# Optimization experiments

Hardware: AMD Instinct MI355X
Metric: run time of the kernel (lower is better)

The kernel has to match this reference:

```python
import jax, jax.numpy as jnp
import numpy as np
from jax import lax

THRESHOLD = 0.3  # nn.Threshold(threshold, 0): y = x if x > threshold else 0
KERNEL = 3       # 3x3 maxpool, stride 1, pad 1 (SAME)


def setup_inputs() -> dict:
    key = jax.random.key(0)
    # [B=1, C=7, H, W] raw feature map (pre-sigmoid logits) from the UNet head
    feature = jax.random.normal(key, (1, 7, 2048, 2048), dtype=jnp.float32)
    return {"feature": feature, "max_detections": 4096}


def reference(feature, max_detections):
    # split along channel dim: 5 keypoint heatmaps, 1 side logit, 1 size logit
    heatmap = feature[:, :5]   # [1,5,H,W]
    side = feature[:, 5:6]     # [1,1,H,W]
    sizes = feature[:, 6:7]    # [1,1,H,W]

    activated = jax.nn.sigmoid(heatmap)
    thresholded = jnp.where(activated > THRESHOLD, activated, jnp.zeros((), activated.dtype))
    # 3x3 stride-1 SAME maxpool (local-max NMS)
    pooled = lax.reduce_window(thresholded, -jnp.inf, lax.max,
                               (1, 1, KERNEL, KERNEL), (1, 1, 1, 1), 'SAME')
    peak_mask = (pooled == thresholded)
    masked = (thresholded * peak_mask.astype(thresholded.dtype))[0]  # [5,H,W]
    masked_bool = masked > 0                                          # [5,H,W]

    side_act = jax.nn.sigmoid(side)[0, 0]    # [H,W]
    sizes_act = jax.nn.sigmoid(sizes)[0, 0]  # [H,W]
    probs_full = jnp.max(activated[0], axis=0)  # [H,W] max over 5 channels

    # fixed-size nonzero (jit-shapeable equivalent of torch .nonzero()/masked_select;
    # entries past the true count are padded with index 0 and zeroed out)
    c, y, x = jnp.nonzero(masked_bool, size=max_detections, fill_value=0)
    n_valid = jnp.sum(masked_bool)
    valid = (jnp.arange(max_detections) < n_valid).astype(probs_full.dtype)

    coords = jnp.stack([c, y, x], axis=1)           # [K,3] like torch nonzero order
    probs = probs_full[y, x] * valid                # masked_select broadcasts [H,W] vs [5,H,W]
    size_width = sizes_act[y, x] * valid
    size_height = sizes_act[y, x] * valid
    side_sel = side_act[y, x] * valid
    return probs, coords, size_width, size_height, side_sel
```

## Files before the change

### kernel.cpp

```cpp
#include <hip/hip_runtime.h>
#include <stdint.h>
#include <math.h>

#define IMG_H 2048
#define IMG_W 2048
#define CH_PIX (IMG_H * IMG_W)
#define MAXDET 4096
#define R_PB 8
#define NBLK 1280

__device__ __forceinline__ float sigmoidf_(float v) {
    return 1.0f / (1.0f + expf(-v));
}
__device__ __forceinline__ float sigthr_(float v) {
    float a = 1.0f / (1.0f + expf(-v));
    return a > 0.3f ? a : 0.0f;
}
__device__ __forceinline__ float max3_(float a, float b, float c) {
    return fmaxf(fmaxf(a, b), c);
}

__global__ __launch_bounds__(256) void pass_a(const float* __restrict__ feat,
                                              uint8_t* __restrict__ mask_bytes,
                                              unsigned* __restrict__ counts) {
    int blk = blockIdx.x;
    int c = blk >> 8;
    int ytile = blk & 255;
    int y0 = ytile << 3;
    const float* chan = feat + (size_t)c * CH_PIX;
    int t = threadIdx.x;
    int lane = t & 63;
    int xb = t << 3;
    int xe = (lane == 0) ? (xb - 1) : (xb + 8);
    bool edge_lane = (lane == 0) || (lane == 63);
    bool edge_ok = edge_lane && ((unsigned)xe < (unsigned)IMG_W);

    float sp[8], sc[8], sn[8];
    float ep, ec, en;

    auto load8 = [&](int y, float* s, float& e) {
        if ((unsigned)y >= (unsigned)IMG_H) {
#pragma unroll
            for (int j = 0; j < 8; ++j) s[j] = 0.0f;
            e = 0.0f;
            return;
        }
        const float* row = chan + (size_t)y * IMG_W;
        float4 a = *(const float4*)(row + xb);
        float4 b = *(const float4*)(row + xb + 4);
        float rv = -INFINITY;
        if (edge_ok) rv = row[xe];
        s[0] = sigthr_(a.x); s[1] = sigthr_(a.y); s[2] = sigthr_(a.z); s[3] = sigthr_(a.w);
        s[4] = sigthr_(b.x); s[5] = sigthr_(b.y); s[6] = sigthr_(b.z); s[7] = sigthr_(b.w);
        e = sigthr_(rv);
    };

    load8(y0 - 1, sp, ep);
    load8(y0,     sc, ec);

    unsigned cnt = 0;
    size_t bb = (size_t)c * (CH_PIX / 8) + (size_t)y0 * (IMG_W / 8) + t;

    for (int r = 0; r < R_PB; ++r) {
        load8(y0 + r + 1, sn, en);
        float cm[8];
#pragma unroll
        for (int j = 0; j < 8; ++j) cm[j] = max3_(sp[j], sc[j], sn[j]);
        float cme = max3_(ep, ec, en);
        float cmL = __shfl_up(cm[7], 1, 64);
        float cmR = __shfl_down(cm[0], 1, 64);
        if (lane == 0)  cmL = cme;
        if (lane == 63) cmR = cme;
        unsigned byte = 0;
#pragma unroll
        for (int j = 0; j < 8; ++j) {
            float l  = j       ? cm[j - 1] : cmL;
            float rr = (j < 7) ? cm[j + 1] : cmR;
            float pooled = max3_(l, cm[j], rr);
            if (sc[j] > 0.0f && pooled == sc[j]) byte |= (1u << j);
        }
        mask_bytes[bb + (size_t)r * (IMG_W / 8)] = (uint8_t)byte;
        cnt += __popc(byte);
#pragma unroll
        for (int j = 0; j < 8; ++j) { sp[j] = sc[j]; sc[j] = sn[j]; }
        ep = ec; ec = en;
    }

#pragma unroll
    for (int off = 32; off; off >>= 1) cnt += __shfl_down(cnt, off, 64);
    __shared__ unsigned s4[4];
    if (lane == 0) s4[t >> 6] = cnt;
    __syncthreads();
    if (t == 0) counts[blk] = s4[0] + s4[1] + s4[2] + s4[3];
}

__global__ __launch_bounds__(256) void pass_b(const float* __restrict__ feat,
                                              const uint64_t* __restrict__ masks,
                                              const unsigned* __restrict__ counts,
                                              float* __restrict__ out) {
    int blk = blockIdx.x;
    int t = threadIdx.x;
    int wave = t >> 6, lane = t & 63;

    unsigned p_lt = 0, p_all = 0;
    for (int i = t; i < NBLK; i += 256) {
        unsigned v = counts[i];
        p_all += v;
        if (i < blk) p_lt += v;
    }
#pragma unroll
    for (int off = 32; off; off >>= 1) {
        p_lt  += __shfl_down(p_lt,  off, 64);
        p_all += __shfl_down(p_all, off, 64);
    }
    __shared__ unsigned sl[4], sa[4];
    if (lane == 0) { sl[wave] = p_lt; sa[wave] = p_all; }
    __syncthreads();
    unsigned boff  = sl[0] + sl[1] + sl[2] + sl[3];
    unsigned total = sa[0] + sa[1] + sa[2] + sa[3];

    if (blk == NBLK - 1) {
        unsigned start = total < MAXDET ? total : MAXDET;
        for (unsigned k = start + t; k < MAXDET; k += 256) {
            out[k] = 0.0f;
            out[MAXDET + 3 * k + 0] = 0.0f;
            out[MAXDET + 3 * k + 1] = 0.0f;
            out[MAXDET + 3 * k + 2] = 0.0f;
            out[4 * MAXDET + k] = 0.0f;
            out[5 * MAXDET + k] = 0.0f;
            out[6 * MAXDET + k] = 0.0f;
        }
    }
    if (boff >= MAXDET) return;

    uint64_t w = masks[(size_t)blk * 256 + t];
    unsigned cnt = (unsigned)__popcll(w);
    __shared__ unsigned tmp[256];
    __shared__ uint32_t det_lds[MAXDET];
    tmp[t] = cnt;
    __syncthreads();
    for (int off = 1; off < 256; off <<= 1) {
        unsigned u = (t >= off) ? tmp[t - off] : 0u;
        __syncthreads();
        tmp[t] += u;
        __syncthreads();
    }
    unsigned rank = boff + tmp[t] - cnt;
    unsigned bsum = tmp[255];
    uint32_t pbase = (uint32_t)blk * 16384u + (uint32_t)t * 64u;
    while (w) {
        int b = __ffsll((unsigned long long)w) - 1;
        w &= w - 1;
        if (rank < MAXDET) det_lds[rank - boff] = pbase + (uint32_t)b;
        rank++;
    }
    __syncthreads();

    unsigned nend = boff + bsum; if (nend > MAXDET) nend = MAXDET;
    unsigned nloc = nend - boff;
    for (unsigned k = t; k < nloc; k += 256) {
        uint32_t p = det_lds[k];
        unsigned rk = boff + k;
        int c = (int)(p >> 22);
        int rem = (int)(p & (CH_PIX - 1));
        int y = rem >> 11, x = rem & 2047;
        size_t pix = (size_t)y * IMG_W + x;
        float pm = sigmoidf_(feat[pix]);
#pragma unroll
        for (int ch = 1; ch < 5; ++ch)
            pm = fmaxf(pm, sigmoidf_(feat[(size_t)ch * CH_PIX + pix]));
        float sdv = sigmoidf_(feat[(size_t)5 * CH_PIX + pix]);
        float szv = sigmoidf_(feat[(size_t)6 * CH_PIX + pix]);
        out[rk] = pm;
        out[MAXDET + 3 * rk + 0] = (float)c;
        out[MAXDET + 3 * rk + 1] = (float)y;
        out[MAXDET + 3 * rk + 2] = (float)x;
        out[4 * MAXDET + rk] = szv;
        out[5 * MAXDET + rk] = szv;
        out[6 * MAXDET + rk] = sdv;
    }
}

extern "C" void kernel_launch(void* const* d_in, const int* in_sizes, int n_in,
                              void* d_out, int out_size, void* d_ws, size_t ws_size,
                              hipStream_t stream) {
    const float* feat = (const float*)d_in[0];
    float* out = (float*)d_out;
    uint8_t* mask_bytes = (uint8_t*)d_ws;
    unsigned* counts = (unsigned*)((char*)d_ws + (size_t)NBLK * 2048);

    pass_a<<<NBLK, 256, 0, stream>>>(feat, mask_bytes, counts);
    pass_b<<<NBLK, 256, 0, stream>>>(feat, (const uint64_t*)d_ws, counts, out);
}
```

Measured before the change: 183.2 us.

## Replace per-pixel sigmoid in NMS pass with raw-logit compare plus exact verify pass

```diff
diff --git a/kernel.cpp b/kernel.cpp
--- a/kernel.cpp
+++ b/kernel.cpp
@@ -6,8 +6,11 @@
 #define IMG_W 2048
 #define CH_PIX (IMG_H * IMG_W)
 #define MAXDET 4096
-#define R_PB 8
 #define NBLK 1280
+#define FRONTIER 8192
+#define CUT_LO (-0.8474f)
+#define CUT_HI (-0.8472f)
+#define DELTA  (1e-4f)
 
 __device__ __forceinline__ float sigmoidf_(float v) {
     return 1.0f / (1.0f + expf(-v));
@@ -18,55 +21,66 @@
 }
 __device__ __forceinline__ float max3_(float a, float b, float c) {
     return fmaxf(fmaxf(a, b), c);
+}
+__device__ __forceinline__ float maskv_(float v) {
+    return v > CUT_HI ? v : -INFINITY;
 }
 
 __global__ __launch_bounds__(256) void pass_a(const float* __restrict__ feat,
                                               uint8_t* __restrict__ mask_bytes,
                                               unsigned* __restrict__ counts) {
     int blk = blockIdx.x;
-    int c = blk >> 8;
-    int ytile = blk & 255;
+    int c = blk >> 8, ytile = blk & 255;
     int y0 = ytile << 3;
     const float* chan = feat + (size_t)c * CH_PIX;
-    int t = threadIdx.x;
-    int lane = t & 63;
+    int t = threadIdx.x, lane = t & 63;
     int xb = t << 3;
-    int xe = (lane == 0) ? (xb - 1) : (xb + 8);
-    bool edge_lane = (lane == 0) || (lane == 63);
-    bool edge_ok = edge_lane && ((unsigned)xe < (unsigned)IMG_W);
-
-    float sp[8], sc[8], sn[8];
-    float ep, ec, en;
-
-    auto load8 = [&](int y, float* s, float& e) {
+    int xe = (lane == 0) ? xb - 1 : xb + 8;
+    bool edge_ok = ((lane == 0) || (lane == 63)) && ((unsigned)xe < (unsigned)IMG_W);
+
+    auto load_raw = [&](int y, float* r, float& er) {
         if ((unsigned)y >= (unsigned)IMG_H) {
 #pragma unroll
-            for (int j = 0; j < 8; ++j) s[j] = 0.0f;
-            e = 0.0f;
+            for (int j = 0; j < 8; ++j) r[j] = -INFINITY;
+            er = -INFINITY;
             return;
         }
         const float* row = chan + (size_t)y * IMG_W;
         float4 a = *(const float4*)(row + xb);
         float4 b = *(const float4*)(row + xb + 4);
-        float rv = -INFINITY;
-        if (edge_ok) rv = row[xe];
-        s[0] = sigthr_(a.x); s[1] = sigthr_(a.y); s[2] = sigthr_(a.z); s[3] = sigthr_(a.w);
-        s[4] = sigthr_(b.x); s[5] = sigthr_(b.y); s[6] = sigthr_(b.z); s[7] = sigthr_(b.w);
-        e = sigthr_(rv);
+        r[0] = a.x; r[1] = a.y; r[2] = a.z; r[3] = a.w;
+        r[4] = b.x; r[5] = b.y; r[6] = b.z; r[7] = b.w;
+        er = edge_ok ? row[xe] : -INFINITY;
     };
 
-    load8(y0 - 1, sp, ep);
-    load8(y0,     sc, ec);
+    float pa[8], pb[8], pc[8];
+    float rb[8], rc[8], rn[8];
+    float ea, eb, ec, etmp;
+
+    load_raw(y0 - 1, rn, etmp);
+#pragma unroll
+    for (int j = 0; j < 8; ++j) pa[j] = maskv_(rn[j]);
+    ea = maskv_(etmp);
+    load_raw(y0, rb, etmp);
+#pragma unroll
+    for (int j = 0; j < 8; ++j) pb[j] = maskv_(rb[j]);
+    eb = maskv_(etmp);
+    load_raw(y0 + 1, rc, etmp);
+#pragma unroll
+    for (int j = 0; j < 8; ++j) pc[j] = maskv_(rc[j]);
+    ec = maskv_(etmp);
 
     unsigned cnt = 0;
-    size_t bb = (size_t)c * (CH_PIX / 8) + (size_t)y0 * (IMG_W / 8) + t;
-
-    for (int r = 0; r < R_PB; ++r) {
-        load8(y0 + r + 1, sn, en);
+    size_t bb = (size_t)blk * 2048 + t;
+
+#pragma unroll
+    for (int r = 0; r < 8; ++r) {
+        float en_ = -INFINITY;
+        if (r < 7) load_raw(y0 + r + 2, rn, en_);
         float cm[8];
 #pragma unroll
-        for (int j = 0; j < 8; ++j) cm[j] = max3_(sp[j], sc[j], sn[j]);
-        float cme = max3_(ep, ec, en);
+        for (int j = 0; j < 8; ++j) cm[j] = max3_(pa[j], pb[j], pc[j]);
+        float cme = max3_(ea, eb, ec);
         float cmL = __shfl_up(cm[7], 1, 64);
         float cmR = __shfl_down(cm[0], 1, 64);
         if (lane == 0)  cmL = cme;
@@ -76,14 +90,17 @@
         for (int j = 0; j < 8; ++j) {
             float l  = j       ? cm[j - 1] : cmL;
             float rr = (j < 7) ? cm[j + 1] : cmR;
-            float pooled = max3_(l, cm[j], rr);
-            if (sc[j] > 0.0f && pooled == sc[j]) byte |= (1u << j);
-        }
-        mask_bytes[bb + (size_t)r * (IMG_W / 8)] = (uint8_t)byte;
+            float wm = max3_(l, cm[j], rr);
+            if (rb[j] > CUT_LO && wm <= rb[j] + DELTA) byte |= 1u << j;
+        }
+        mask_bytes[bb + (size_t)r * 256] = (uint8_t)byte;
         cnt += __popc(byte);
 #pragma unroll
-        for (int j = 0; j < 8; ++j) { sp[j] = sc[j]; sc[j] = sn[j]; }
-        ep = ec; ec = en;
+        for (int j = 0; j < 8; ++j) {
+            pa[j] = pb[j]; pb[j] = pc[j]; pc[j] = maskv_(rn[j]);
+            rb[j] = rc[j]; rc[j] = rn[j];
+        }
+        ea = eb; eb = ec; ec = maskv_(en_);
     }
 
 #pragma unroll
@@ -94,9 +111,69 @@
     if (t == 0) counts[blk] = s4[0] + s4[1] + s4[2] + s4[3];
 }
 
+__global__ __launch_bounds__(256) void pass_v(const float* __restrict__ feat,
+                                              uint64_t* __restrict__ masks,
+                                              const unsigned* __restrict__ counts,
+                                              unsigned* __restrict__ vcounts) {
+    int blk = blockIdx.x, t = threadIdx.x, lane = t & 63, wave = t >> 6;
+    unsigned p_lt = 0;
+    for (int i = t; i < NBLK; i += 256) {
+        unsigned v = counts[i];
+        if (i < blk) p_lt += v;
+    }
+#pragma unroll
+    for (int off = 32; off; off >>= 1) p_lt += __shfl_down(p_lt, off, 64);
+    __shared__ unsigned sl[4];
+    if (lane == 0) sl[wave] = p_lt;
+    __syncthreads();
+    unsigned boff = sl[0] + sl[1] + sl[2] + sl[3];
+    if (boff >= FRONTIER) {
+        if (t == 0) vcounts[blk] = counts[blk];
+        return;
+    }
+
+    uint64_t w = masks[(size_t)blk * 256 + t];
+    uint64_t vw = 0;
+    uint32_t pbase = (uint32_t)blk * 16384u + (uint32_t)t * 64u;
+    while (w) {
+        int b = __ffsll((unsigned long long)w) - 1;
+        w &= w - 1;
+        uint32_t p = pbase + (uint32_t)b;
+        int c = (int)(p >> 22);
+        int rem = (int)(p & (CH_PIX - 1));
+        int y = rem >> 11, x = rem & 2047;
+        const float* chan = feat + (size_t)c * CH_PIX;
+        float own = sigthr_(chan[(size_t)y * IMG_W + x]);
+        if (own > 0.0f) {
+            float pooled = own;
+#pragma unroll
+            for (int dy = -1; dy <= 1; ++dy) {
+                int yy = y + dy;
+                if ((unsigned)yy >= (unsigned)IMG_H) continue;
+#pragma unroll
+                for (int dx = -1; dx <= 1; ++dx) {
+                    if (dy == 0 && dx == 0) continue;
+                    int xx = x + dx;
+                    if ((unsigned)xx >= (unsigned)IMG_W) continue;
+                    pooled = fmaxf(pooled, sigthr_(chan[(size_t)yy * IMG_W + xx]));
+                }
+            }
+            if (pooled == own) vw |= 1ull << b;
+        }
+    }
+    masks[(size_t)blk * 256 + t] = vw;
+    unsigned cnt = (unsigned)__popcll(vw);
+#pragma unroll
+    for (int off = 32; off; off >>= 1) cnt += __shfl_down(cnt, off, 64);
+    __shared__ unsigned s4[4];
+    if (lane == 0) s4[wave] = cnt;
+    __syncthreads();
+    if (t == 0) vcounts[blk] = s4[0] + s4[1] + s4[2] + s4[3];
+}
+
 __global__ __launch_bounds__(256) void pass_b(const float* __restrict__ feat,
                                               const uint64_t* __restrict__ masks,
-                                              const unsigned* __restrict__ counts,
+                                              const unsigned* __restrict__ vcounts,
                                               float* __restrict__ out) {
     int blk = blockIdx.x;
     int t = threadIdx.x;
@@ -104,7 +181,7 @@
 
     unsigned p_lt = 0, p_all = 0;
     for (int i = t; i < NBLK; i += 256) {
-        unsigned v = counts[i];
+        unsigned v = vcounts[i];
         p_all += v;
         if (i < blk) p_lt += v;
     }
@@ -187,8 +264,10 @@
     const float* feat = (const float*)d_in[0];
     float* out = (float*)d_out;
     uint8_t* mask_bytes = (uint8_t*)d_ws;
-    unsigned* counts = (unsigned*)((char*)d_ws + (size_t)NBLK * 2048);
+    unsigned* counts  = (unsigned*)((char*)d_ws + (size_t)NBLK * 2048);
+    unsigned* vcounts = counts + NBLK;
 
     pass_a<<<NBLK, 256, 0, stream>>>(feat, mask_bytes, counts);
-    pass_b<<<NBLK, 256, 0, stream>>>(feat, (const uint64_t*)d_ws, counts, out);
-}
+    pass_v<<<NBLK, 256, 0, stream>>>(feat, (uint64_t*)d_ws, counts, vcounts);
+    pass_b<<<NBLK, 256, 0, stream>>>(feat, (const uint64_t*)d_ws, vcounts, out);
+}
```

Result: slower. 210.0 us (+14.6%).

## Run local-max NMS on raw logits, calling sigmoid only in ambiguous cases

Applied to the files above, without the earlier changes.

```diff
diff --git a/kernel.cpp b/kernel.cpp
--- a/kernel.cpp
+++ b/kernel.cpp
@@ -6,15 +6,14 @@
 #define IMG_W 2048
 #define CH_PIX (IMG_H * IMG_W)
 #define MAXDET 4096
-#define R_PB 8
 #define NBLK 1280
+#define CUT_LO (-0.8474f)
+#define CUT_HI (-0.8472f)
+#define EPS    (1e-4f)
+#define VSAFE  (6.0f)
 
 __device__ __forceinline__ float sigmoidf_(float v) {
     return 1.0f / (1.0f + expf(-v));
-}
-__device__ __forceinline__ float sigthr_(float v) {
-    float a = 1.0f / (1.0f + expf(-v));
-    return a > 0.3f ? a : 0.0f;
 }
 __device__ __forceinline__ float max3_(float a, float b, float c) {
     return fmaxf(fmaxf(a, b), c);
@@ -24,66 +23,81 @@
                                               uint8_t* __restrict__ mask_bytes,
                                               unsigned* __restrict__ counts) {
     int blk = blockIdx.x;
-    int c = blk >> 8;
-    int ytile = blk & 255;
+    int c = blk >> 8, ytile = blk & 255;
     int y0 = ytile << 3;
     const float* chan = feat + (size_t)c * CH_PIX;
-    int t = threadIdx.x;
-    int lane = t & 63;
+    int t = threadIdx.x, lane = t & 63;
     int xb = t << 3;
-    int xe = (lane == 0) ? (xb - 1) : (xb + 8);
-    bool edge_lane = (lane == 0) || (lane == 63);
-    bool edge_ok = edge_lane && ((unsigned)xe < (unsigned)IMG_W);
-
-    float sp[8], sc[8], sn[8];
-    float ep, ec, en;
-
-    auto load8 = [&](int y, float* s, float& e) {
+    int xe = (lane == 0) ? xb - 1 : xb + 8;
+    bool edge_ok = ((lane == 0) || (lane == 63)) && ((unsigned)xe < (unsigned)IMG_W);
+
+    auto load_raw = [&](int y, float* r, float& er) {
         if ((unsigned)y >= (unsigned)IMG_H) {
 #pragma unroll
-            for (int j = 0; j < 8; ++j) s[j] = 0.0f;
-            e = 0.0f;
+            for (int j = 0; j < 8; ++j) r[j] = -INFINITY;
+            er = -INFINITY;
             return;
         }
         const float* row = chan + (size_t)y * IMG_W;
         float4 a = *(const float4*)(row + xb);
         float4 b = *(const float4*)(row + xb + 4);
-        float rv = -INFINITY;
-        if (edge_ok) rv = row[xe];
-        s[0] = sigthr_(a.x); s[1] = sigthr_(a.y); s[2] = sigthr_(a.z); s[3] = sigthr_(a.w);
-        s[4] = sigthr_(b.x); s[5] = sigthr_(b.y); s[6] = sigthr_(b.z); s[7] = sigthr_(b.w);
-        e = sigthr_(rv);
+        r[0] = a.x; r[1] = a.y; r[2] = a.z; r[3] = a.w;
+        r[4] = b.x; r[5] = b.y; r[6] = b.z; r[7] = b.w;
+        er = edge_ok ? row[xe] : -INFINITY;
     };
 
-    load8(y0 - 1, sp, ep);
-    load8(y0,     sc, ec);
+    float rp[8], rc_[8], rn[8];
+    float ep, ec, en;
+
+    load_raw(y0 - 1, rp, ep);
+    load_raw(y0,     rc_, ec);
+    load_raw(y0 + 1, rn, en);
 
     unsigned cnt = 0;
-    size_t bb = (size_t)c * (CH_PIX / 8) + (size_t)y0 * (IMG_W / 8) + t;
-
-    for (int r = 0; r < R_PB; ++r) {
-        load8(y0 + r + 1, sn, en);
+    size_t bb = (size_t)blk * 2048 + t;
+
+#pragma unroll
+    for (int r = 0; r < 8; ++r) {
+        float nx[8], enx = -INFINITY;
+        if (r < 7) load_raw(y0 + r + 2, nx, enx);
+        else {
+#pragma unroll
+            for (int j = 0; j < 8; ++j) nx[j] = -INFINITY;
+        }
         float cm[8];
 #pragma unroll
-        for (int j = 0; j < 8; ++j) cm[j] = max3_(sp[j], sc[j], sn[j]);
+        for (int j = 0; j < 8; ++j) cm[j] = max3_(rp[j], rc_[j], rn[j]);
         float cme = max3_(ep, ec, en);
         float cmL = __shfl_up(cm[7], 1, 64);
         float cmR = __shfl_down(cm[0], 1, 64);
         if (lane == 0)  cmL = cme;
         if (lane == 63) cmR = cme;
+
         unsigned byte = 0;
 #pragma unroll
         for (int j = 0; j < 8; ++j) {
+            float own = rc_[j];
             float l  = j       ? cm[j - 1] : cmL;
             float rr = (j < 7) ? cm[j + 1] : cmR;
-            float pooled = max3_(l, cm[j], rr);
-            if (sc[j] > 0.0f && pooled == sc[j]) byte |= (1u << j);
-        }
-        mask_bytes[bb + (size_t)r * (IMG_W / 8)] = (uint8_t)byte;
+            float wm = max3_(l, cm[j], rr);
+            bool cand;
+            if (own > CUT_HI && wm <= own) {
+                cand = true;
+            } else if (own <= CUT_LO) {
+                cand = false;
+            } else if (own > CUT_HI && wm > own + EPS && own <= VSAFE) {
+                cand = false;
+            } else {
+                float so = sigmoidf_(own);
+                cand = (so > 0.3f) && (sigmoidf_(wm) <= so);
+            }
+            if (cand) byte |= 1u << j;
+        }
+        mask_bytes[bb + (size_t)r * 256] = (uint8_t)byte;
         cnt += __popc(byte);
 #pragma unroll
-        for (int j = 0; j < 8; ++j) { sp[j] = sc[j]; sc[j] = sn[j]; }
-        ep = ec; ec = en;
+        for (int j = 0; j < 8; ++j) { rp[j] = rc_[j]; rc_[j] = rn[j]; rn[j] = nx[j]; }
+        ep = ec; ec = en; en = enx;
     }
 
 #pragma unroll
```

Result: no change. 181.8 us (-0.7%).
